# Kernel tuning notes

Hardware: AMD Instinct MI355X
Metric: run time of the kernel (lower is better)

## Reference

```python
import jax, jax.numpy as jnp
import numpy as np

B, T, IN, H = 1024, 256, 2, 128
H1, H2, H3 = H // 2, H, 2 * H


def _param(key, shape, fan):
    bound = 1.0 / np.sqrt(fan)
    return jax.random.uniform(key, shape, jnp.float32, -bound, bound)


def setup_inputs() -> dict:
    key = jax.random.key(0)
    ks = jax.random.split(key, 16)
    inp = {
        "input": jax.random.normal(ks[0], (B, T, IN), jnp.float32),
        "future": 16,
        # LSTMCell 1: in=IN, hid=H1 (torch gate order i,f,g,o)
        "W_ih1": _param(ks[1], (4 * H1, IN), H1),
        "W_hh1": _param(ks[2], (4 * H1, H1), H1),
        "b_ih1": _param(ks[3], (4 * H1,), H1),
        "b_hh1": _param(ks[4], (4 * H1,), H1),
        # LSTMCell 2: in=H1, hid=H2
        "W_ih2": _param(ks[5], (4 * H2, H1), H2),
        "W_hh2": _param(ks[6], (4 * H2, H2), H2),
        "b_ih2": _param(ks[7], (4 * H2,), H2),
        "b_hh2": _param(ks[8], (4 * H2,), H2),
        # LSTMCell 3: in=H2, hid=H3
        "W_ih3": _param(ks[9], (4 * H3, H2), H3),
        "W_hh3": _param(ks[10], (4 * H3, H3), H3),
        "b_ih3": _param(ks[11], (4 * H3,), H3),
        "b_hh3": _param(ks[12], (4 * H3,), H3),
        # Linear: (H1+H2+H3) -> IN
        "W_lin": _param(ks[13], (IN, H1 + H2 + H3), H1 + H2 + H3),
        "b_lin": _param(ks[14], (IN,), H1 + H2 + H3),
    }
    return inp


def _lstm_cell(x, h, c, Wih, Whh, bih, bhh):
    g = x @ Wih.T + h @ Whh.T + (bih + bhh)
    i, f, gg, o = jnp.split(g, 4, axis=-1)
    c_new = jax.nn.sigmoid(f) * c + jax.nn.sigmoid(i) * jnp.tanh(gg)
    h_new = jax.nn.sigmoid(o) * jnp.tanh(c_new)
    return h_new, c_new


def reference(input, future, W_ih1, W_hh1, b_ih1, b_hh1,
              W_ih2, W_hh2, b_ih2, b_hh2,
              W_ih3, W_hh3, b_ih3, b_hh3, W_lin, b_lin):
    b = input.shape[0]

    def step(state, x):
        h1, c1, h2, c2, h3, c3 = state
        h1, c1 = _lstm_cell(x, h1, c1, W_ih1, W_hh1, b_ih1, b_hh1)
        h2, c2 = _lstm_cell(h1, h2, c2, W_ih2, W_hh2, b_ih2, b_hh2)
        h3, c3 = _lstm_cell(h2, h3, c3, W_ih3, W_hh3, b_ih3, b_hh3)
        out = jnp.concatenate([h1, h2, h3], axis=-1) @ W_lin.T + b_lin
        return (h1, c1, h2, c2, h3, c3), out

    z = lambda d: jnp.zeros((b, d), input.dtype)
    state0 = (z(H1), z(H1), z(H2), z(H2), z(H3), z(H3))

    # consume the input sequence; only the last output is kept (as in torch code)
    def scan_step(state, x):
        state, out = step(state, x)
        return state, out

    state, outs = jax.lax.scan(scan_step, state0, input.transpose(1, 0, 2))
    out = outs[-1]  # [B, IN]

    def fstep(carry, _):
        state, out = carry
        state, out2 = step(state, out)
        return (state, out2), out2

    (_, _), fouts = jax.lax.scan(fstep, (state, out), None, length=future - 1)
    # stack: first kept output + generated ones -> [B, future, IN]
    return jnp.concatenate([out[:, None, :], fouts.transpose(1, 0, 2)], axis=1)
```

## Files before the change

kernel.cpp:

```cpp
#include <hip/hip_runtime.h>


#define T_SEQ 256
#define NTEAM 32
#define DEPTH 8
#define DMASK 7

#define NJT1 4
#define NJT2 8
#define NJT3 16
#define NKB1 3
#define NKB2 6
#define NKB3 12

#define WSZ1 (NJT1*4*NKB1*512)
#define WSZ2 (NJT2*4*NKB2*512)
#define WSZ3 (NJT3*4*NKB3*512)
#define WTOT (WSZ1+WSZ2+WSZ3)

#define H2_G    2048
#define H2_SLOT (2*H2_G)
#define H2_TEAM (DEPTH*H2_SLOT)
#define H3_G    4096
#define H3_SLOT (2*H3_G)
#define H3_TEAM (DEPTH*H3_SLOT)
#define CAP_WAIT (1<<21)

typedef _Float16 half8 __attribute__((ext_vector_type(8)));
typedef _Float16 half4 __attribute__((ext_vector_type(4)));
typedef float f32x4 __attribute__((ext_vector_type(4)));

__device__ __forceinline__ float sigm(float x) {
  return __fdividef(1.f, 1.f + __expf(-x));
}
__device__ __forceinline__ float tanh_fast(float x) {
  float t = __expf(-2.f * fabsf(x));
  float r = __fdividef(1.f - t, 1.f + t);
  return copysignf(r, x);
}

__device__ __forceinline__ void ldg16(half8* d, const _Float16* p) {
  asm volatile("global_load_dwordx4 %0, %1, off sc0 sc1"
               : "=v"(*d) : "v"(p) : "memory");
}
__device__ __forceinline__ void stg8(_Float16* p, half4 v) {
  asm volatile("global_store_dwordx2 %0, %1, off sc0 sc1"
               :: "v"(p), "v"(v) : "memory");
}
__device__ __forceinline__ void drain() {
  asm volatile("s_waitcnt vmcnt(0)" ::: "memory");
  __builtin_amdgcn_sched_barrier(0);
}
__device__ __forceinline__ void stflag(int* p, int v) {
  __hip_atomic_store(p, v, __ATOMIC_RELAXED, __HIP_MEMORY_SCOPE_SYSTEM);
}
__device__ __forceinline__ void wait_team(const int* fb, int t3, int tf,
                                          volatile int* sdead) {
  if (*sdead) return;
  const int lane = threadIdx.x & 63;
  const int* p = fb + ((lane < 5) ? lane : 0) * 64;
  const int tg = (lane < 4) ? t3 : (lane == 4 ? tf : (int)0x80000000);
  int iter = 0;
  while (true) {
    const int v = __hip_atomic_load(p, __ATOMIC_RELAXED, __HIP_MEMORY_SCOPE_SYSTEM);
    if (__all(v >= tg)) break;
    if (++iter > CAP_WAIT) { if (lane == 0) *sdead = 1; break; }
    __builtin_amdgcn_s_sleep(1);
  }
  asm volatile("" ::: "memory");
}

__global__ void prep_weights(const float* __restrict__ Wih1, const float* __restrict__ Whh1,
                             const float* __restrict__ Wih2, const float* __restrict__ Whh2,
                             const float* __restrict__ Wih3, const float* __restrict__ Whh3,
                             _Float16* __restrict__ WT) {
  int idx = blockIdx.x * blockDim.x + threadIdx.x;
  if (idx >= WTOT) return;
  float v = 0.f;
  if (idx < WSZ1) {
    const int e = idx, blk = e >> 9, wb = e & 511;
    const int lane = wb >> 3, j = wb & 7;
    const int tl = blk / NKB1, kk = blk % NKB1;
    const int q = tl / NJT1, jt = tl % NJT1;
    const int r = q * 64 + jt * 16 + (lane & 15);
    const int k = kk * 32 + ((lane >> 4) << 3) + j;
    if (k < 64)       v = Whh1[r * 64 + k];
    else if (k < 66)  v = Wih1[r * 2 + (k - 64)];
  } else if (idx < WSZ1 + WSZ2) {
    const int e = idx - WSZ1, blk = e >> 9, wb = e & 511;
    const int lane = wb >> 3, j = wb & 7;
    const int tl = blk / NKB2, kk = blk % NKB2;
    const int q = tl / NJT2, jt = tl % NJT2;
    const int r = q * 128 + jt * 16 + (lane & 15);
    const int k = kk * 32 + ((lane >> 4) << 3) + j;
    if (k < 64)       v = Wih2[r * 64 + k];
    else              v = Whh2[r * 128 + (k - 64)];
  } else {
    const int e = idx - WSZ1 - WSZ2, blk = e >> 9, wb = e & 511;
    const int lane = wb >> 3, j = wb & 7;
    const int tl = blk / NKB3, kk = blk % NKB3;
    const int q = tl / NJT3, jt = tl % NJT3;
    const int r = q * 256 + jt * 16 + (lane & 15);
    const int k = kk * 32 + ((lane >> 4) << 3) + j;
    if (k < 128)      v = Wih3[r * 128 + k];
    else              v = Whh3[r * 256 + (k - 128)];
  }
  WT[idx] = (_Float16)v;
}

__global__ __launch_bounds__(256, 1) void pipe_main(
    const float* __restrict__ input, const int* __restrict__ future_p,
    const float* __restrict__ bih1, const float* __restrict__ bhh1,
    const float* __restrict__ bih2, const float* __restrict__ bhh2,
    const float* __restrict__ bih3, const float* __restrict__ bhh3,
    const float* __restrict__ Wlin, const float* __restrict__ blin,
    const _Float16* __restrict__ WT,
    _Float16* __restrict__ h2r, _Float16* __restrict__ h3r,
    int* __restrict__ flags,
    float* __restrict__ out) {
  __shared__ __align__(16) _Float16 xh1s[2][16][104];
  __shared__ __align__(16) _Float16 xh2s[2][16][200];
  __shared__ __align__(16) _Float16 xh3ld[2][16][264];
  __shared__ float wlin[2][448];
  __shared__ volatile int sh_dead;

  const int fut = *future_p;
  const int nsteps = T_SEQ - 1 + fut;

  const int team = blockIdx.x & 31;
  const int role = blockIdx.x >> 5;
  const int b0 = team * 32;
  const int NEG = (int)0x80000000;

  int* fb = flags + team * 512;
  _Float16* h2b = h2r + (size_t)team * H2_TEAM;
  _Float16* h3b = h3r + (size_t)team * H3_TEAM;

  const int tid = threadIdx.x;
  const int w = tid >> 6, lane = tid & 63;
  const int n = lane & 15, l4 = lane >> 4;
  if (tid == 0) sh_dead = 0;

  if (role == 0) {
    for (int i = tid; i < 2*16*104; i += 256) (&xh1s[0][0][0])[i] = (_Float16)0.f;
    for (int i = tid; i < 2*16*200; i += 256) (&xh2s[0][0][0])[i] = (_Float16)0.f;
    for (int i = tid; i < 896; i += 256) (&wlin[0][0])[i] = Wlin[i];

    half8 a1[4][3];
#pragma unroll
    for (int q = 0; q < 4; ++q)
#pragma unroll
      for (int kk = 0; kk < 3; ++kk)
        a1[q][kk] = *(const half8*)(WT + ((q*NJT1 + w)*NKB1 + kk)*512 + lane*8);
    half8 a2[2][4][6];
#pragma unroll
    for (int u = 0; u < 2; ++u)
#pragma unroll
      for (int q = 0; q < 4; ++q)
#pragma unroll
        for (int kk = 0; kk < 6; ++kk)
          a2[u][q][kk] = *(const half8*)(WT + WSZ1 + ((q*NJT2 + (u*4+w))*NKB2 + kk)*512 + lane*8);
    float b1r[4][4], b2r[2][4][4];
#pragma unroll
    for (int q = 0; q < 4; ++q)
#pragma unroll
      for (int e = 0; e < 4; ++e) {
        const int r1 = q*64 + w*16 + l4*4 + e;
        b1r[q][e] = bih1[r1] + bhh1[r1];
#pragma unroll
        for (int u = 0; u < 2; ++u) {
          const int r2 = q*128 + (u*4+w)*16 + l4*4 + e;
          b2r[u][q][e] = bih2[r2] + bhh2[r2];
        }
      }
    float c1[2][4] = {}, c2[2][2][4] = {};
    __syncthreads();

    for (int it = 0; it <= nsteps; ++it) {
      const int tp = it - 1;
      wait_team(fb, (it >= T_SEQ) ? it : it - 6, NEG, &sh_dead);

      if (tp >= T_SEQ - 1) {
        const _Float16* src = h3b + (size_t)(tp & DMASK) * H3_SLOT;
        half8 tmp[4];
#pragma unroll
        for (int i = 0; i < 4; ++i) ldg16(&tmp[i], src + (tid + i*256)*8);
        drain();
#pragma unroll
        for (int i = 0; i < 4; ++i) {
          const int idx = tid + i*256;
          const int gl = idx >> 9, nn = (idx >> 5) & 15, c = (idx & 31) * 8;
          *(half8*)(&xh3ld[gl][nn][c]) = tmp[i];
        }
        __syncthreads();
        if (tid < 128) {
          const int kq = tid & 1, ch = (tid >> 1) & 1, nn = (tid >> 2) & 15, gl = (tid >> 6) & 1;
          float acc = 0.f;
#pragma unroll
          for (int i = 0; i < 56; ++i) {
            const int k = kq*224 + i*4;
            const half4 xv = (k < 192) ? *(const half4*)(&xh2s[gl][nn][k])
                                       : *(const half4*)(&xh3ld[gl][nn][k - 192]);
            const float* wl = &wlin[ch][k];
            acc = fmaf(wl[0], (float)xv[0], acc);
            acc = fmaf(wl[1], (float)xv[1], acc);
            acc = fmaf(wl[2], (float)xv[2], acc);
            acc = fmaf(wl[3], (float)xv[3], acc);
          }
          acc += __shfl_xor(acc, 1, 64);
          if (kq == 0) {
            const float o = acc + blin[ch];
            out[((size_t)(b0 + gl*16 + nn)*fut + (tp - (T_SEQ - 1)))*2 + ch] = o;
            xh1s[gl][nn][64 + ch] = (_Float16)o;
          }
        }
      }
      if (it < T_SEQ && tid < 64) {
        const int gl = tid >> 5, nn = (tid >> 1) & 15, ch = tid & 1;
        xh1s[gl][nn][64 + ch] =
            (_Float16)input[((size_t)(b0 + gl*16 + nn)*T_SEQ + it)*2 + ch];
      }
      __syncthreads();
      if (it == nsteps) break;

      half8 bf1[2][3];
#pragma unroll
      for (int g = 0; g < 2; ++g)
#pragma unroll
        for (int kk = 0; kk < 3; ++kk)
          bf1[g][kk] = *(const half8*)(&xh1s[g][n][kk*32 + l4*8]);
      __syncthreads();
#pragma unroll
      for (int g = 0; g < 2; ++g) {
        f32x4 acc[4];
#pragma unroll
        for (int q = 0; q < 4; ++q)
#pragma unroll
          for (int e = 0; e < 4; ++e) acc[q][e] = b1r[q][e];
#pragma unroll
        for (int q = 0; q < 4; ++q)
#pragma unroll
          for (int kk = 0; kk < 3; ++kk)
            acc[q] = __builtin_amdgcn_mfma_f32_16x16x32_f16(a1[q][kk], bf1[g][kk], acc[q], 0, 0, 0);
        half4 hv;
#pragma unroll
        for (int e = 0; e < 4; ++e) {
          const float cn = sigm(acc[1][e]) * c1[g][e] + sigm(acc[0][e]) * tanh_fast(acc[2][e]);
          const float h = sigm(acc[3][e]) * tanh_fast(cn);
          c1[g][e] = cn;
          hv[e] = (_Float16)h;
        }
        *(half4*)(&xh1s[g][n][w*16 + l4*4]) = hv;
        *(half4*)(&xh2s[g][n][w*16 + l4*4]) = hv;
      }
      __syncthreads();

      half8 bf2[2][6];
#pragma unroll
      for (int g = 0; g < 2; ++g)
#pragma unroll
        for (int kk = 0; kk < 6; ++kk)
          bf2[g][kk] = *(const half8*)(&xh2s[g][n][kk*32 + l4*8]);
      __syncthreads();
      const int slot = it & DMASK;
#pragma unroll
      for (int u = 0; u < 2; ++u)
#pragma unroll
        for (int g = 0; g < 2; ++g) {
          f32x4 acc[4];
#pragma unroll
          for (int q = 0; q < 4; ++q)
#pragma unroll
            for (int e = 0; e < 4; ++e) acc[q][e] = b2r[u][q][e];
#pragma unroll
          for (int q = 0; q < 4; ++q)
#pragma unroll
            for (int kk = 0; kk < 6; ++kk)
              acc[q] = __builtin_amdgcn_mfma_f32_16x16x32_f16(a2[u][q][kk], bf2[g][kk], acc[q], 0, 0, 0);
          half4 hv;
#pragma unroll
          for (int e = 0; e < 4; ++e) {
            const float cn = sigm(acc[1][e]) * c2[u][g][e] + sigm(acc[0][e]) * tanh_fast(acc[2][e]);
            const float h = sigm(acc[3][e]) * tanh_fast(cn);
            c2[u][g][e] = cn;
            hv[e] = (_Float16)h;
          }
          const int row = (u*4 + w)*16 + l4*4;
          *(half4*)(&xh2s[g][n][64 + row]) = hv;
          stg8(h2b + (size_t)slot*H2_SLOT + g*H2_G + n*128 + row, hv);
        }
      asm volatile("s_waitcnt vmcnt(0)" ::: "memory");
      __syncthreads();
      if (tid == 0) stflag(fb + 4*64, it + 1);
    }
  } else {
    const int slice = role - 1;
    const int tl = slice*4 + w;
    half8 a3[4][12];
#pragma unroll
    for (int q = 0; q < 4; ++q)
#pragma unroll
      for (int kk = 0; kk < 12; ++kk)
        a3[q][kk] = *(const half8*)(WT + WSZ1 + WSZ2 + ((q*NJT3 + tl)*NKB3 + kk)*512 + lane*8);
    float b3r[4][4];
#pragma unroll
    for (int q = 0; q < 4; ++q)
#pragma unroll
      for (int e = 0; e < 4; ++e) {
        const int r = q*256 + tl*16 + l4*4 + e;
        b3r[q][e] = bih3[r] + bhh3[r];
      }
    float c3[2][4] = {};
    __syncthreads();

    for (int t = 0; t < nsteps; ++t) {
      wait_team(fb, t, t + 1, &sh_dead);
      const int slot = t & DMASK, slot1 = (t - 1) & DMASK;
      half8 bf[2][12];
#pragma unroll
      for (int g = 0; g < 2; ++g) {
        const _Float16* h2p = h2b + (size_t)slot*H2_SLOT + g*H2_G + n*128;
#pragma unroll
        for (int kk = 0; kk < 4; ++kk) ldg16(&bf[g][kk], h2p + kk*32 + l4*8);
      }
      if (t > 0) {
#pragma unroll
        for (int g = 0; g < 2; ++g) {
          const _Float16* h3p = h3b + (size_t)slot1*H3_SLOT + g*H3_G + n*256;
#pragma unroll
          for (int kk = 4; kk < 12; ++kk) ldg16(&bf[g][kk], h3p + (kk-4)*32 + l4*8);
        }
      } else {
#pragma unroll
        for (int g = 0; g < 2; ++g)
#pragma unroll
          for (int kk = 4; kk < 12; ++kk) bf[g][kk] = half8{};
      }
      drain();
#pragma unroll
      for (int g = 0; g < 2; ++g) {
        f32x4 acc[4];
#pragma unroll
        for (int q = 0; q < 4; ++q)
#pragma unroll
          for (int e = 0; e < 4; ++e) acc[q][e] = b3r[q][e];
#pragma unroll
        for (int q = 0; q < 4; ++q)
#pragma unroll
          for (int kk = 0; kk < 12; ++kk)
            acc[q] = __builtin_amdgcn_mfma_f32_16x16x32_f16(a3[q][kk], bf[g][kk], acc[q], 0, 0, 0);
        half4 hv;
#pragma unroll
        for (int e = 0; e < 4; ++e) {
          const float cn = sigm(acc[1][e]) * c3[g][e] + sigm(acc[0][e]) * tanh_fast(acc[2][e]);
          const float h = sigm(acc[3][e]) * tanh_fast(cn);
          c3[g][e] = cn;
          hv[e] = (_Float16)h;
        }
        stg8(h3b + (size_t)slot*H3_SLOT + g*H3_G + n*256 + tl*16 + l4*4, hv);
      }
      asm volatile("s_waitcnt vmcnt(0)" ::: "memory");
      __syncthreads();
      if (tid == 0) stflag(fb + slice*64, t + 1);
    }
  }
}

extern "C" void kernel_launch(void* const* d_in, const int* in_sizes, int n_in,
                              void* d_out, int out_size, void* d_ws, size_t ws_size,
                              hipStream_t stream) {
  const float* input = (const float*)d_in[0];
  const int*   fut   = (const int*)d_in[1];
  const float* Wih1  = (const float*)d_in[2];
  const float* Whh1  = (const float*)d_in[3];
  const float* bih1  = (const float*)d_in[4];
  const float* bhh1  = (const float*)d_in[5];
  const float* Wih2  = (const float*)d_in[6];
  const float* Whh2  = (const float*)d_in[7];
  const float* bih2  = (const float*)d_in[8];
  const float* bhh2  = (const float*)d_in[9];
  const float* Wih3  = (const float*)d_in[10];
  const float* Whh3  = (const float*)d_in[11];
  const float* bih3  = (const float*)d_in[12];
  const float* bhh3  = (const float*)d_in[13];
  const float* Wlin  = (const float*)d_in[14];
  const float* blin  = (const float*)d_in[15];
  float* out = (float*)d_out;

  _Float16* WT  = (_Float16*)d_ws;
  _Float16* h2r = WT + WTOT;
  _Float16* h3r = h2r + (size_t)NTEAM * H2_TEAM;
  int* flags    = (int*)(h3r + (size_t)NTEAM * H3_TEAM);
  const size_t flag_bytes = (size_t)NTEAM * 512 * sizeof(int);

  prep_weights<<<(WTOT + 255) / 256, 256, 0, stream>>>(Wih1, Whh1, Wih2, Whh2, Wih3, Whh3, WT);
  hipMemsetAsync(flags, 0, flag_bytes, stream);
  pipe_main<<<5 * NTEAM, 256, 0, stream>>>(input, fut,
                                           bih1, bhh1, bih2, bhh2, bih3, bhh3,
                                           Wlin, blin, WT, h2r, h3r, flags, out);
}
```

Before: 1.862 ms.

## Replace per-block barrier+flag with per-wave progress flags in LSTM pipeline

After: 1.880 ms. No clear change (+1.0%).

```diff
diff --git a/kernel.cpp b/kernel.cpp
--- a/kernel.cpp
+++ b/kernel.cpp
@@ -24,6 +24,7 @@
 #define H3_G    4096
 #define H3_SLOT (2*H3_G)
 #define H3_TEAM (DEPTH*H3_SLOT)
+#define FL_TEAM 2048
 #define CAP_WAIT (1<<21)
 
 typedef _Float16 half8 __attribute__((ext_vector_type(8)));
@@ -54,17 +55,30 @@
 __device__ __forceinline__ void stflag(int* p, int v) {
   __hip_atomic_store(p, v, __ATOMIC_RELAXED, __HIP_MEMORY_SCOPE_SYSTEM);
 }
-__device__ __forceinline__ void wait_team(const int* fb, int t3, int tf,
-                                          volatile int* sdead) {
-  if (*sdead) return;
+__device__ __forceinline__ void wait16(const int* fb, int tg3, int* dead) {
+  if (*dead) return;
   const int lane = threadIdx.x & 63;
-  const int* p = fb + ((lane < 5) ? lane : 0) * 64;
-  const int tg = (lane < 4) ? t3 : (lane == 4 ? tf : (int)0x80000000);
+  const int* p = fb + ((lane < 16) ? lane : 0) * 64;
+  const int tg = (lane < 16) ? tg3 : (int)0x80000000;
   int iter = 0;
   while (true) {
     const int v = __hip_atomic_load(p, __ATOMIC_RELAXED, __HIP_MEMORY_SCOPE_SYSTEM);
     if (__all(v >= tg)) break;
-    if (++iter > CAP_WAIT) { if (lane == 0) *sdead = 1; break; }
+    if (++iter > CAP_WAIT) { *dead = 1; break; }
+    __builtin_amdgcn_s_sleep(1);
+  }
+  asm volatile("" ::: "memory");
+}
+__device__ __forceinline__ void wait20(const int* fb, int t3, int tf, int* dead) {
+  if (*dead) return;
+  const int lane = threadIdx.x & 63;
+  const int* p = fb + ((lane < 20) ? lane : 0) * 64;
+  const int tg = (lane < 16) ? t3 : (lane < 20 ? tf : (int)0x80000000);
+  int iter = 0;
+  while (true) {
+    const int v = __hip_atomic_load(p, __ATOMIC_RELAXED, __HIP_MEMORY_SCOPE_SYSTEM);
+    if (__all(v >= tg)) break;
+    if (++iter > CAP_WAIT) { *dead = 1; break; }
     __builtin_amdgcn_s_sleep(1);
   }
   asm volatile("" ::: "memory");
@@ -122,7 +136,6 @@
   __shared__ __align__(16) _Float16 xh2s[2][16][200];
   __shared__ __align__(16) _Float16 xh3ld[2][16][264];
   __shared__ float wlin[2][448];
-  __shared__ volatile int sh_dead;
 
   const int fut = *future_p;
   const int nsteps = T_SEQ - 1 + fut;
@@ -130,16 +143,15 @@
   const int team = blockIdx.x & 31;
   const int role = blockIdx.x >> 5;
   const int b0 = team * 32;
-  const int NEG = (int)0x80000000;
-
-  int* fb = flags + team * 512;
+
+  int* fb = flags + team * FL_TEAM;
   _Float16* h2b = h2r + (size_t)team * H2_TEAM;
   _Float16* h3b = h3r + (size_t)team * H3_TEAM;
 
   const int tid = threadIdx.x;
   const int w = tid >> 6, lane = tid & 63;
   const int n = lane & 15, l4 = lane >> 4;
-  if (tid == 0) sh_dead = 0;
+  int dead = 0;
 
   if (role == 0) {
     for (int i = tid; i < 2*16*104; i += 256) (&xh1s[0][0][0])[i] = (_Float16)0.f;
@@ -178,7 +190,7 @@
 
     for (int it = 0; it <= nsteps; ++it) {
       const int tp = it - 1;
-      wait_team(fb, (it >= T_SEQ) ? it : it - 6, NEG, &sh_dead);
+      wait16(fb, (it >= T_SEQ) ? it : it - 6, &dead);
 
       if (tp >= T_SEQ - 1) {
         const _Float16* src = h3b + (size_t)(tp & DMASK) * H3_SLOT;
@@ -290,8 +302,8 @@
           stg8(h2b + (size_t)slot*H2_SLOT + g*H2_G + n*128 + row, hv);
         }
       asm volatile("s_waitcnt vmcnt(0)" ::: "memory");
+      if (lane == 0) stflag(fb + (16 + w)*64, it + 1);
       __syncthreads();
-      if (tid == 0) stflag(fb + 4*64, it + 1);
     }
   } else {
     const int slice = role - 1;
@@ -311,10 +323,10 @@
         b3r[q][e] = bih3[r] + bhh3[r];
       }
     float c3[2][4] = {};
-    __syncthreads();
 
     for (int t = 0; t < nsteps; ++t) {
-      wait_team(fb, t, t + 1, &sh_dead);
+      if (dead) break;
+      wait20(fb, t, t + 1, &dead);
       const int slot = t & DMASK, slot1 = (t - 1) & DMASK;
       half8 bf[2][12];
 #pragma unroll
@@ -360,8 +372,7 @@
         stg8(h3b + (size_t)slot*H3_SLOT + g*H3_G + n*256 + tl*16 + l4*4, hv);
       }
       asm volatile("s_waitcnt vmcnt(0)" ::: "memory");
-      __syncthreads();
-      if (tid == 0) stflag(fb + slice*64, t + 1);
+      if (lane == 0) stflag(fb + tl*64, t + 1);
     }
   }
 }
@@ -391,7 +402,7 @@
   _Float16* h2r = WT + WTOT;
   _Float16* h3r = h2r + (size_t)NTEAM * H2_TEAM;
   int* flags    = (int*)(h3r + (size_t)NTEAM * H3_TEAM);
-  const size_t flag_bytes = (size_t)NTEAM * 512 * sizeof(int);
+  const size_t flag_bytes = (size_t)NTEAM * FL_TEAM * sizeof(int);
 
   prep_weights<<<(WTOT + 255) / 256, 256, 0, stream>>>(Wih1, Whh1, Wih2, Whh2, Wih3, Whh3, WT);
   hipMemsetAsync(flags, 0, flag_bytes, stream);
```
